# Kernel optimization log

Measured on AMD Instinct MI355X. Metric: run time of the kernel, lower is better.

Reference implementation:

```python
import jax, jax.numpy as jnp
import numpy as np

HIDDEN = 4096
NUM_HEADS = 32
HEAD_DIM = HIDDEN // NUM_HEADS  # 128, also rotary_dim
SCALING = HEAD_DIM ** -0.5
ROPE_BASE = 10000.0
B, S = 2, 2048


def apply_rope(x, positions):
    # x: [B, S, H, D], positions: [B, S] int
    half = HEAD_DIM // 2
    inv_freq = 1.0 / (ROPE_BASE ** (jnp.arange(0, half, dtype=jnp.float32) / half))
    angles = positions.astype(jnp.float32)[..., None] * inv_freq  # [B, S, half]
    cos = jnp.cos(angles)[:, :, None, :]  # [B, S, 1, half]
    sin = jnp.sin(angles)[:, :, None, :]
    x1, x2 = x[..., :half], x[..., half:]
    return jnp.concatenate([x1 * cos - x2 * sin, x2 * cos + x1 * sin], axis=-1)


def setup_inputs() -> dict:
    key = jax.random.key(0)
    k1, k2, k3 = jax.random.split(key, 3)
    hidden_states = jax.random.normal(k1, (B, S, HIDDEN), dtype=jnp.float32)
    W_qkv = jax.random.normal(k2, (HIDDEN, 3 * HIDDEN), dtype=jnp.float32) * (HIDDEN ** -0.5)
    W_o = jax.random.normal(k3, (HIDDEN, HIDDEN), dtype=jnp.float32) * (HIDDEN ** -0.5)
    positions = jnp.broadcast_to(jnp.arange(S, dtype=jnp.int32), (B, S))
    return {"positions": positions, "hidden_states": hidden_states, "W_qkv": W_qkv, "W_o": W_o}


def reference(positions, hidden_states, W_qkv, W_o):
    qkv = hidden_states @ W_qkv  # [B, S, 3*HIDDEN]
    q, k, v = jnp.split(qkv, 3, axis=-1)
    q = q.reshape(B, S, NUM_HEADS, HEAD_DIM)
    k = k.reshape(B, S, NUM_HEADS, HEAD_DIM)
    v = v.reshape(B, S, NUM_HEADS, HEAD_DIM)
    q = apply_rope(q, positions)
    k = apply_rope(k, positions)
    scores = jnp.einsum('bqhd,bkhd->bhqk', q, k) * SCALING
    causal = jnp.tril(jnp.ones((S, S), dtype=bool))
    scores = jnp.where(causal[None, None], scores, jnp.finfo(scores.dtype).min)
    probs = jax.nn.softmax(scores, axis=-1)
    attn = jnp.einsum('bhqk,bkhd->bqhd', probs, v).reshape(B, S, HIDDEN)
    return attn @ W_o
```

## Files before the change

kernel.cpp:

```cpp
#include <hip/hip_runtime.h>
#include <math.h>

typedef unsigned int uint;
typedef unsigned short ushort;

#define HID   4096
#define N3    12288
#define NH    32
#define HD    128
#define SEQ   2048
#define BATCH 2
#define MROWS 4096

typedef __attribute__((ext_vector_type(4))) float  f32x4;
typedef __attribute__((ext_vector_type(8))) short  bf16x8;
typedef __attribute__((ext_vector_type(4))) ushort u16x4;

static __device__ __forceinline__ ushort f2bf(float f) {
    uint u = __builtin_bit_cast(uint, f);
    u += 0x7fffu + ((u >> 16) & 1u);
    return (ushort)(u >> 16);
}
static __device__ __forceinline__ float bf2f(ushort s) {
    uint u = ((uint)s) << 16;
    return __builtin_bit_cast(float, u);
}
static __device__ __forceinline__ uint pack2(float a, float b) {
    return (uint)f2bf(a) | ((uint)f2bf(b) << 16);
}

template<int A_BF16, int OUT_BF16>
__global__ __launch_bounds__(256) void gemm_kernel(
    const void* __restrict__ Ap, const float* __restrict__ Bw,
    void* __restrict__ Cp, int K, int lda, int ldb, int ldc)
{
    __shared__ __align__(16) ushort Alds[128 * 40];
    __shared__ __align__(16) ushort Blds[128 * 40];

    const int tid = threadIdx.x;
    const int w = tid >> 6, l = tid & 63, c = l & 15, G = l >> 4;
    const int wr = w >> 1, wc = w & 1;
    const int m0 = blockIdx.y * 128, n0 = blockIdx.x * 128;

    f32x4 acc[4][4];
#pragma unroll
    for (int mi = 0; mi < 4; ++mi)
#pragma unroll
        for (int ni = 0; ni < 4; ++ni)
            acc[mi][ni] = (f32x4){0.f, 0.f, 0.f, 0.f};

    for (int k0 = 0; k0 < K; k0 += 32) {
#pragma unroll
        for (int i = 0; i < 2; ++i) {
            int seg = i * 256 + tid;
            int m = seg >> 2, kk = (seg & 3) * 8;
            if (A_BF16) {
                const ushort* ap = (const ushort*)Ap + (size_t)(m0 + m) * lda + k0 + kk;
                *(uint4*)&Alds[m * 40 + kk] = *(const uint4*)ap;
            } else {
                const float* ap = (const float*)Ap + (size_t)(m0 + m) * lda + k0 + kk;
                float4 f0 = *(const float4*)ap;
                float4 f1 = *(const float4*)(ap + 4);
                uint4 v;
                v.x = pack2(f0.x, f0.y); v.y = pack2(f0.z, f0.w);
                v.z = pack2(f1.x, f1.y); v.w = pack2(f1.z, f1.w);
                *(uint4*)&Alds[m * 40 + kk] = v;
            }
        }
#pragma unroll
        for (int i = 0; i < 2; ++i) {
            int seg = i * 256 + tid;
            int kk = seg >> 4, nn = (seg & 15) * 8;
            const float* bp = Bw + (size_t)(k0 + kk) * ldb + n0 + nn;
            float4 f0 = *(const float4*)bp;
            float4 f1 = *(const float4*)(bp + 4);
            int ebase = (((kk >> 3) ^ ((nn >> 3) & 3)) << 3) + (kk & 7);
            Blds[(nn + 0) * 40 + ebase] = f2bf(f0.x);
            Blds[(nn + 1) * 40 + ebase] = f2bf(f0.y);
            Blds[(nn + 2) * 40 + ebase] = f2bf(f0.z);
            Blds[(nn + 3) * 40 + ebase] = f2bf(f0.w);
            Blds[(nn + 4) * 40 + ebase] = f2bf(f1.x);
            Blds[(nn + 5) * 40 + ebase] = f2bf(f1.y);
            Blds[(nn + 6) * 40 + ebase] = f2bf(f1.z);
            Blds[(nn + 7) * 40 + ebase] = f2bf(f1.w);
        }
        __syncthreads();

        bf16x8 af[4], bf[4];
#pragma unroll
        for (int mi = 0; mi < 4; ++mi)
            af[mi] = *(const bf16x8*)&Alds[(wr * 64 + mi * 16 + c) * 40 + 8 * G];
#pragma unroll
        for (int ni = 0; ni < 4; ++ni) {
            int n = wc * 64 + ni * 16 + c;
            int blk = G ^ ((n >> 3) & 3);
            bf[ni] = *(const bf16x8*)&Blds[n * 40 + blk * 8];
        }
#pragma unroll
        for (int mi = 0; mi < 4; ++mi)
#pragma unroll
            for (int ni = 0; ni < 4; ++ni)
                acc[mi][ni] = __builtin_amdgcn_mfma_f32_16x16x32_bf16(
                    af[mi], bf[ni], acc[mi][ni], 0, 0, 0);
        __syncthreads();
    }

#pragma unroll
    for (int mi = 0; mi < 4; ++mi)
#pragma unroll
        for (int ni = 0; ni < 4; ++ni) {
            int row = m0 + wr * 64 + mi * 16 + 4 * G;
            int col = n0 + wc * 64 + ni * 16 + c;
#pragma unroll
            for (int r_ = 0; r_ < 4; ++r_) {
                if (OUT_BF16)
                    ((ushort*)Cp)[(size_t)(row + r_) * ldc + col] = f2bf(acc[mi][ni][r_]);
                else
                    ((float*)Cp)[(size_t)(row + r_) * ldc + col] = acc[mi][ni][r_];
            }
        }
}

__global__ __launch_bounds__(256) void rope_kernel(ushort* qkv, const int* __restrict__ pos)
{
    int tid = blockIdx.x * 256 + threadIdx.x;
    int d  = tid & 63;
    int h  = (tid >> 6) & 31;
    int qk = (tid >> 11) & 1;
    int r  = tid >> 12;
    float p = (float)pos[r];
    float inv = exp2f(-0.20762050593296276f * (float)d);
    float ang = p * inv;
    float sn, cs;
    sincosf(ang, &sn, &cs);
    ushort* base = qkv + (size_t)r * N3 + qk * HID + h * HD + d;
    float x1 = bf2f(base[0]);
    float x2 = bf2f(base[64]);
    base[0]  = f2bf(x1 * cs - x2 * sn);
    base[64] = f2bf(x2 * cs + x1 * sn);
}

__global__ __launch_bounds__(256) void attn_kernel(ushort* qkv)
{
    __shared__ __align__(16) ushort Klds[64 * 136];
    __shared__ __align__(16) ushort Vt[128 * 72];
    __shared__ __align__(16) ushort Plds[4 * 16 * 72];

    const int qt = blockIdx.x, h = blockIdx.y, b = blockIdx.z;
    const int tid = threadIdx.x;
    const int w = tid >> 6, l = tid & 63, c = l & 15, G = l >> 4;
    const float SC2 = 0.08838834764831845f * 1.4426950408889634f;

    const ushort* Qp = qkv + (size_t)(b * SEQ + qt * 64 + w * 16 + c) * N3 + h * HD;
    bf16x8 qf[4];
#pragma unroll
    for (int kc = 0; kc < 4; ++kc)
        qf[kc] = *(const bf16x8*)(Qp + kc * 32 + 8 * G);

    f32x4 o[8];
#pragma unroll
    for (int nd = 0; nd < 8; ++nd) o[nd] = (f32x4){0.f, 0.f, 0.f, 0.f};
    float mrun[4] = {-INFINITY, -INFINITY, -INFINITY, -INFINITY};
    float lrun[4] = {0.f, 0.f, 0.f, 0.f};

    const ushort* Kbase = qkv + (size_t)b * SEQ * N3 + HID + h * HD;
    const ushort* Vbase = qkv + (size_t)b * SEQ * N3 + 2 * HID + h * HD;

    for (int t = 0; t <= qt; ++t) {
        int kv0 = t * 64;
#pragma unroll
        for (int i = 0; i < 4; ++i) {
            int seg = i * 256 + tid;
            int r = seg >> 4, c0 = (seg & 15) * 8;
            uint4 kvv = *(const uint4*)(Kbase + (size_t)(kv0 + r) * N3 + c0);
            *(uint4*)&Klds[r * 136 + c0] = kvv;
        }
        {
            int r0 = (tid >> 4) * 4;
            int c0 = (tid & 15) * 8;
            union { uint4 v; ushort s[8]; } va, vb, vc, vd;
            va.v = *(const uint4*)(Vbase + (size_t)(kv0 + r0 + 0) * N3 + c0);
            vb.v = *(const uint4*)(Vbase + (size_t)(kv0 + r0 + 1) * N3 + c0);
            vc.v = *(const uint4*)(Vbase + (size_t)(kv0 + r0 + 2) * N3 + c0);
            vd.v = *(const uint4*)(Vbase + (size_t)(kv0 + r0 + 3) * N3 + c0);
#pragma unroll
            for (int j = 0; j < 8; ++j) {
                int d = c0 + j;
                int blk = (r0 >> 3) ^ ((d >> 3) & 7);
                u16x4 pk = {va.s[j], vb.s[j], vc.s[j], vd.s[j]};
                *(u16x4*)&Vt[d * 72 + blk * 8 + (r0 & 7)] = pk;
            }
        }
        __syncthreads();

        f32x4 sc[4];
#pragma unroll
        for (int nf = 0; nf < 4; ++nf) sc[nf] = (f32x4){0.f, 0.f, 0.f, 0.f};
#pragma unroll
        for (int nf = 0; nf < 4; ++nf)
#pragma unroll
            for (int kc = 0; kc < 4; ++kc) {
                bf16x8 kf = *(const bf16x8*)&Klds[(16 * nf + c) * 136 + 32 * kc + 8 * G];
                sc[nf] = __builtin_amdgcn_mfma_f32_16x16x32_bf16(qf[kc], kf, sc[nf], 0, 0, 0);
            }

        if (t == qt) {
#pragma unroll
            for (int nf = 0; nf < 4; ++nf)
#pragma unroll
                for (int r_ = 0; r_ < 4; ++r_)
                    if (16 * nf + c > w * 16 + 4 * G + r_)
                        sc[nf][r_] = -INFINITY;
        }

        float alpha[4];
        float p[4][4];
#pragma unroll
        for (int r_ = 0; r_ < 4; ++r_) {
            float pm = fmaxf(fmaxf(sc[0][r_], sc[1][r_]), fmaxf(sc[2][r_], sc[3][r_]));
#pragma unroll
            for (int msk = 1; msk < 16; msk <<= 1)
                pm = fmaxf(pm, __shfl_xor(pm, msk, 64));
            float mnew = fmaxf(mrun[r_], pm);
            float al = exp2f((mrun[r_] - mnew) * SC2);
            float rs = 0.f;
#pragma unroll
            for (int nf = 0; nf < 4; ++nf) {
                float pv = exp2f((sc[nf][r_] - mnew) * SC2);
                pv = bf2f(f2bf(pv));
                p[nf][r_] = pv;
                rs += pv;
            }
#pragma unroll
            for (int msk = 1; msk < 16; msk <<= 1)
                rs += __shfl_xor(rs, msk, 64);
            lrun[r_] = lrun[r_] * al + rs;
            mrun[r_] = mnew;
            alpha[r_] = al;
        }
#pragma unroll
        for (int nd = 0; nd < 8; ++nd)
#pragma unroll
            for (int r_ = 0; r_ < 4; ++r_)
                o[nd][r_] *= alpha[r_];

#pragma unroll
        for (int nf = 0; nf < 4; ++nf)
#pragma unroll
            for (int r_ = 0; r_ < 4; ++r_)
                Plds[w * 1152 + (4 * G + r_) * 72 + 16 * nf + c] = f2bf(p[nf][r_]);

#pragma unroll
        for (int kc2 = 0; kc2 < 2; ++kc2) {
            bf16x8 pa = *(const bf16x8*)&Plds[w * 1152 + c * 72 + 32 * kc2 + 8 * G];
#pragma unroll
            for (int nd = 0; nd < 8; ++nd) {
                int dn = 16 * nd + c;
                int blk = (4 * kc2 + G) ^ ((dn >> 3) & 7);
                bf16x8 vb = *(const bf16x8*)&Vt[dn * 72 + blk * 8];
                o[nd] = __builtin_amdgcn_mfma_f32_16x16x32_bf16(pa, vb, o[nd], 0, 0, 0);
            }
        }
        __syncthreads();
    }

    float inv[4];
#pragma unroll
    for (int r_ = 0; r_ < 4; ++r_) inv[r_] = 1.0f / lrun[r_];
    ushort* Op = qkv + (size_t)(b * SEQ + qt * 64 + w * 16) * N3 + h * HD;
#pragma unroll
    for (int nd = 0; nd < 8; ++nd)
#pragma unroll
        for (int r_ = 0; r_ < 4; ++r_)
            Op[(size_t)(4 * G + r_) * N3 + 16 * nd + c] = f2bf(o[nd][r_] * inv[r_]);
}

extern "C" void kernel_launch(void* const* d_in, const int* in_sizes, int n_in,
                              void* d_out, int out_size, void* d_ws, size_t ws_size,
                              hipStream_t stream)
{
    const int*   positions = (const int*)d_in[0];
    const float* hidden    = (const float*)d_in[1];
    const float* Wqkv      = (const float*)d_in[2];
    const float* Wo        = (const float*)d_in[3];
    ushort* qkv = (ushort*)d_ws;

    dim3 blk(256);
    gemm_kernel<0, 1><<<dim3(N3 / 128, MROWS / 128), blk, 0, stream>>>(
        hidden, Wqkv, qkv, HID, HID, N3, N3);
    rope_kernel<<<dim3((MROWS * 2 * NH * 64) / 256), blk, 0, stream>>>(qkv, positions);
    attn_kernel<<<dim3(SEQ / 64, NH, BATCH), blk, 0, stream>>>(qkv);
    gemm_kernel<1, 0><<<dim3(HID / 128, MROWS / 128), blk, 0, stream>>>(
        qkv, Wo, (float*)d_out, HID, N3, HID, HID);
    (void)in_sizes; (void)n_in; (void)out_size; (void)ws_size;
}
```

Baseline: 1.886 ms.

## Pre-convert operands to bf16 and use direct global-to-LDS loads in GEMMs

Adds separate kernels that convert hidden states to bf16 and transpose-convert each weight matrix to a K-major bf16 layout in workspace. The GEMM then loads both operands with global_load_lds 16-byte transfers straight into LDS, with a K-step of 64 instead of 32. This removes the in-loop fp32-to-bf16 conversion and the scattered 2-byte LDS writes, and halves the number of barriers per K. The cost is extra conversion and transpose passes over the weights each call, and unpadded LDS rows that may cause bank conflicts.

```diff
diff --git a/kernel.cpp b/kernel.cpp
--- a/kernel.cpp
+++ b/kernel.cpp
@@ -28,14 +28,54 @@
 static __device__ __forceinline__ uint pack2(float a, float b) {
     return (uint)f2bf(a) | ((uint)f2bf(b) << 16);
 }
-
-template<int A_BF16, int OUT_BF16>
-__global__ __launch_bounds__(256) void gemm_kernel(
-    const void* __restrict__ Ap, const float* __restrict__ Bw,
+static __device__ __forceinline__ void gld_lds16(const ushort* g, ushort* l) {
+    __builtin_amdgcn_global_load_lds(
+        (const __attribute__((address_space(1))) void*)g,
+        (__attribute__((address_space(3))) void*)l, 16, 0, 0);
+}
+
+__global__ __launch_bounds__(256) void conv_f32_bf16(
+    const float* __restrict__ src, ushort* __restrict__ dst)
+{
+    size_t i = ((size_t)blockIdx.x * 256 + threadIdx.x) * 8;
+    float4 f0 = *(const float4*)&src[i];
+    float4 f1 = *(const float4*)&src[i + 4];
+    uint4 v;
+    v.x = pack2(f0.x, f0.y); v.y = pack2(f0.z, f0.w);
+    v.z = pack2(f1.x, f1.y); v.w = pack2(f1.z, f1.w);
+    *(uint4*)&dst[i] = v;
+}
+
+__global__ __launch_bounds__(256) void transpose_conv(
+    const float* __restrict__ W, ushort* __restrict__ Wt, int Ncols, int Krows)
+{
+    __shared__ float T[64][65];
+    const int n0 = blockIdx.x * 64, k0 = blockIdx.y * 64;
+    const int tc = (threadIdx.x & 15) * 4, tr = threadIdx.x >> 4;
+#pragma unroll
+    for (int i = 0; i < 4; ++i) {
+        float4 v = *(const float4*)&W[(size_t)(k0 + tr + i * 16) * Ncols + n0 + tc];
+        T[tr + i * 16][tc + 0] = v.x; T[tr + i * 16][tc + 1] = v.y;
+        T[tr + i * 16][tc + 2] = v.z; T[tr + i * 16][tc + 3] = v.w;
+    }
+    __syncthreads();
+    const int on = threadIdx.x >> 2;
+    const int ok = (threadIdx.x & 3) * 16;
+    ushort tmp[16];
+#pragma unroll
+    for (int j = 0; j < 16; ++j) tmp[j] = f2bf(T[ok + j][on]);
+    ushort* out = Wt + (size_t)(n0 + on) * Krows + k0 + ok;
+    *(uint4*)out       = *(uint4*)&tmp[0];
+    *(uint4*)(out + 8) = *(uint4*)&tmp[8];
+}
+
+template<int OUT_BF16>
+__global__ __launch_bounds__(256) void gemm_tn(
+    const ushort* __restrict__ A, const ushort* __restrict__ Bt,
     void* __restrict__ Cp, int K, int lda, int ldb, int ldc)
 {
-    __shared__ __align__(16) ushort Alds[128 * 40];
-    __shared__ __align__(16) ushort Blds[128 * 40];
+    __shared__ __align__(16) ushort Alds[128 * 64];
+    __shared__ __align__(16) ushort Blds[128 * 64];
 
     const int tid = threadIdx.x;
     const int w = tid >> 6, l = tid & 63, c = l & 15, G = l >> 4;
@@ -49,59 +89,40 @@
         for (int ni = 0; ni < 4; ++ni)
             acc[mi][ni] = (f32x4){0.f, 0.f, 0.f, 0.f};
 
-    for (int k0 = 0; k0 < K; k0 += 32) {
-#pragma unroll
-        for (int i = 0; i < 2; ++i) {
-            int seg = i * 256 + tid;
-            int m = seg >> 2, kk = (seg & 3) * 8;
-            if (A_BF16) {
-                const ushort* ap = (const ushort*)Ap + (size_t)(m0 + m) * lda + k0 + kk;
-                *(uint4*)&Alds[m * 40 + kk] = *(const uint4*)ap;
-            } else {
-                const float* ap = (const float*)Ap + (size_t)(m0 + m) * lda + k0 + kk;
-                float4 f0 = *(const float4*)ap;
-                float4 f1 = *(const float4*)(ap + 4);
-                uint4 v;
-                v.x = pack2(f0.x, f0.y); v.y = pack2(f0.z, f0.w);
-                v.z = pack2(f1.x, f1.y); v.w = pack2(f1.z, f1.w);
-                *(uint4*)&Alds[m * 40 + kk] = v;
-            }
-        }
-#pragma unroll
-        for (int i = 0; i < 2; ++i) {
-            int seg = i * 256 + tid;
-            int kk = seg >> 4, nn = (seg & 15) * 8;
-            const float* bp = Bw + (size_t)(k0 + kk) * ldb + n0 + nn;
-            float4 f0 = *(const float4*)bp;
-            float4 f1 = *(const float4*)(bp + 4);
-            int ebase = (((kk >> 3) ^ ((nn >> 3) & 3)) << 3) + (kk & 7);
-            Blds[(nn + 0) * 40 + ebase] = f2bf(f0.x);
-            Blds[(nn + 1) * 40 + ebase] = f2bf(f0.y);
-            Blds[(nn + 2) * 40 + ebase] = f2bf(f0.z);
-            Blds[(nn + 3) * 40 + ebase] = f2bf(f0.w);
-            Blds[(nn + 4) * 40 + ebase] = f2bf(f1.x);
-            Blds[(nn + 5) * 40 + ebase] = f2bf(f1.y);
-            Blds[(nn + 6) * 40 + ebase] = f2bf(f1.z);
-            Blds[(nn + 7) * 40 + ebase] = f2bf(f1.w);
-        }
+    const int srow = w * 32 + (l >> 3);
+    const int selem = (l & 7) * 8;
+    const ushort* Ag = A + (size_t)(m0 + srow) * lda + selem;
+    const ushort* Bg = Bt + (size_t)(n0 + srow) * ldb + selem;
+    ushort* Al = &Alds[(w * 32) * 64];
+    ushort* Bl = &Blds[(w * 32) * 64];
+
+    for (int k0 = 0; k0 < K; k0 += 64) {
+#pragma unroll
+        for (int i = 0; i < 4; ++i)
+            gld_lds16(Ag + k0 + (size_t)i * 8 * lda, Al + i * 8 * 64);
+#pragma unroll
+        for (int i = 0; i < 4; ++i)
+            gld_lds16(Bg + k0 + (size_t)i * 8 * ldb, Bl + i * 8 * 64);
         __syncthreads();
 
-        bf16x8 af[4], bf[4];
-#pragma unroll
-        for (int mi = 0; mi < 4; ++mi)
-            af[mi] = *(const bf16x8*)&Alds[(wr * 64 + mi * 16 + c) * 40 + 8 * G];
-#pragma unroll
-        for (int ni = 0; ni < 4; ++ni) {
-            int n = wc * 64 + ni * 16 + c;
-            int blk = G ^ ((n >> 3) & 3);
-            bf[ni] = *(const bf16x8*)&Blds[n * 40 + blk * 8];
-        }
-#pragma unroll
-        for (int mi = 0; mi < 4; ++mi)
+        bf16x8 af[2][4], bfr[2][4];
+#pragma unroll
+        for (int kk = 0; kk < 2; ++kk) {
+#pragma unroll
+            for (int mi = 0; mi < 4; ++mi)
+                af[kk][mi] = *(const bf16x8*)&Alds[(wr * 64 + mi * 16 + c) * 64 + kk * 32 + 8 * G];
 #pragma unroll
             for (int ni = 0; ni < 4; ++ni)
-                acc[mi][ni] = __builtin_amdgcn_mfma_f32_16x16x32_bf16(
-                    af[mi], bf[ni], acc[mi][ni], 0, 0, 0);
+                bfr[kk][ni] = *(const bf16x8*)&Blds[(wc * 64 + ni * 16 + c) * 64 + kk * 32 + 8 * G];
+        }
+#pragma unroll
+        for (int kk = 0; kk < 2; ++kk)
+#pragma unroll
+            for (int mi = 0; mi < 4; ++mi)
+#pragma unroll
+                for (int ni = 0; ni < 4; ++ni)
+                    acc[mi][ni] = __builtin_amdgcn_mfma_f32_16x16x32_bf16(
+                        af[kk][mi], bfr[kk][ni], acc[mi][ni], 0, 0, 0);
         __syncthreads();
     }
 
@@ -283,14 +304,20 @@
     const float* hidden    = (const float*)d_in[1];
     const float* Wqkv      = (const float*)d_in[2];
     const float* Wo        = (const float*)d_in[3];
+
     ushort* qkv = (ushort*)d_ws;
+    ushort* Abf = (ushort*)((char*)d_ws + 100663296);
+    ushort* Wt  = (ushort*)((char*)d_ws + 134217728);
 
     dim3 blk(256);
-    gemm_kernel<0, 1><<<dim3(N3 / 128, MROWS / 128), blk, 0, stream>>>(
-        hidden, Wqkv, qkv, HID, HID, N3, N3);
+    conv_f32_bf16<<<dim3((MROWS * HID) / (8 * 256)), blk, 0, stream>>>(hidden, Abf);
+    transpose_conv<<<dim3(N3 / 64, HID / 64), blk, 0, stream>>>(Wqkv, Wt, N3, HID);
+    gemm_tn<1><<<dim3(N3 / 128, MROWS / 128), blk, 0, stream>>>(
+        Abf, Wt, qkv, HID, HID, HID, N3);
     rope_kernel<<<dim3((MROWS * 2 * NH * 64) / 256), blk, 0, stream>>>(qkv, positions);
     attn_kernel<<<dim3(SEQ / 64, NH, BATCH), blk, 0, stream>>>(qkv);
-    gemm_kernel<1, 0><<<dim3(HID / 128, MROWS / 128), blk, 0, stream>>>(
-        qkv, Wo, (float*)d_out, HID, N3, HID, HID);
-    (void)in_sizes; (void)n_in; (void)out_size; (void)ws_size;
-}
+    transpose_conv<<<dim3(HID / 64, HID / 64), blk, 0, stream>>>(Wo, Wt, HID, HID);
+    gemm_tn<0><<<dim3(HID / 128, MROWS / 128), blk, 0, stream>>>(
+        qkv, Wt, (float*)d_out, HID, N3, HID, HID);
+    (void)positions; (void)in_sizes; (void)n_in; (void)out_size; (void)ws_size;
+}
```

Result: faster. 1.591 ms (-15.6%).
